# Optimization experiments

Hardware: AMD Instinct MI355X
Metric: run time of the kernel (lower is better)

Reference implementation:

```python
import jax, jax.numpy as jnp
import numpy as np

N_FACTORS = (50, 50, 50)   # vocab factorization, prod = 125000
EMB_STD = (0.5 / 512) ** (1.0 / 3.0)   # per-core std so full embedding std ~= 0.5/embedding_dim
CTX_STD = (1e-6) ** (1.0 / 3.0)


def _tt_gather(core1, core2, core3, idx):
    """idx: flat int array (N,). Cores: (n_k, r_in, m_k, r_out). Returns (N, m1*m2*m3)."""
    n1, n2, n3 = N_FACTORS
    i3 = idx % n3
    i2 = (idx // n3) % n2
    i1 = idx // (n2 * n3)
    N = idx.shape[0]
    g1 = core1[i1][:, 0]                  # (N, m1, r1)  (leading rank is 1)
    g2 = core2[i2]                        # (N, r1, m2, r2)
    res = jnp.einsum('bmr,brns->bmns', g1, g2).reshape(N, -1, g2.shape[-1])  # (N, m1*m2, r2)
    g3 = core3[i3]                        # (N, r2, m3, 1)
    res = jnp.einsum('bmr,brns->bmns', res, g3).reshape(N, -1)               # (N, m1*m2*m3)
    return res


def setup_inputs() -> dict:
    key = jax.random.key(0)
    ks = jax.random.split(key, 8)
    vocab = 125000
    word_indices = jax.random.randint(ks[0], (8192, 1), 0, vocab, dtype=jnp.int64 if jax.config.jax_enable_x64 else jnp.int32)
    context_indices = jax.random.randint(ks[1], (8192, 10), 0, vocab, dtype=jnp.int64 if jax.config.jax_enable_x64 else jnp.int32)
    w_core1 = jax.random.normal(ks[2], (50, 1, 8, 32), dtype=jnp.float32) * EMB_STD
    w_core2 = jax.random.normal(ks[3], (50, 32, 8, 32), dtype=jnp.float32) * EMB_STD
    w_core3 = jax.random.normal(ks[4], (50, 32, 8, 1), dtype=jnp.float32) * EMB_STD
    c_core1 = jax.random.normal(ks[5], (50, 1, 8, 32), dtype=jnp.float32) * CTX_STD
    c_core2 = jax.random.normal(ks[6], (50, 32, 8, 32), dtype=jnp.float32) * CTX_STD
    c_core3 = jax.random.normal(ks[7], (50, 32, 8, 1), dtype=jnp.float32) * CTX_STD
    return {
        'word_indices': word_indices,
        'context_indices': context_indices,
        'w_core1': w_core1, 'w_core2': w_core2, 'w_core3': w_core3,
        'c_core1': c_core1, 'c_core2': c_core2, 'c_core3': c_core3,
    }


def reference(word_indices, context_indices, w_core1, w_core2, w_core3, c_core1, c_core2, c_core3):
    # w = self.w_emb.forward(word_indices)[:, 0, :]
    w = _tt_gather(w_core1, w_core2, w_core3, word_indices[:, 0])          # (B, 512)
    # context_indices is 2-D: flatten, lookup, reshape back
    bs, num = context_indices.shape
    c = _tt_gather(c_core1, c_core2, c_core3, context_indices.reshape(-1)) # (B*num, 512)
    c = c.reshape(bs, num, -1)
    return (w, c)
```

## Files before the change

### kernel.cpp

```cpp
#include <hip/hip_runtime.h>


#define NFAC 50
#define TPAIR 2048
#define NPAIRS 2500
#define NKEYS 5000
#define MAXC 192
#define NWORD 8192
#define NCTX  81920
#define NLOOK (NWORD + NCTX)
#define NBB   ((NLOOK + 255) / 256)

typedef short short8 __attribute__((ext_vector_type(8)));
typedef float f32x4v __attribute__((ext_vector_type(4)));

__device__ __forceinline__ unsigned short f2bf(float f) {
    unsigned u = __builtin_bit_cast(unsigned, f);
    u += 0x7FFFu + ((u >> 16) & 1u);
    return (unsigned short)(u >> 16);
}

__device__ __forceinline__ int pair_of(int idx) {
    const int i3 = idx % NFAC;
    const int i2 = (idx / NFAC) % NFAC;
    return i2 * NFAC + i3;
}


__global__ __launch_bounds__(256) void tt_bucket(
    const int* __restrict__ widx, const int* __restrict__ cidx,
    const float* __restrict__ w1, const float* __restrict__ c1,
    int* __restrict__ hist, unsigned* __restrict__ bucket,
    unsigned short* __restrict__ g1w, unsigned short* __restrict__ g1c)
{
    const int b = blockIdx.x;
    if (b >= NBB) {
        const int g = (b - NBB) * 256 + threadIdx.x;
        if (g < 12800) g1w[g] = f2bf(w1[g]);
        else if (g < 25600) g1c[g - 12800] = f2bf(c1[g - 12800]);
        return;
    }
    const int g = b * 256 + threadIdx.x;
    const int idx = (g < NWORD) ? widx[g] : cidx[g - NWORD];
    const int key = (g < NWORD ? 0 : NPAIRS) + pair_of(idx);
    const int i1  = idx / (NFAC * NFAC);
    const int pos = atomicAdd(&hist[key], 1);
    if (pos < MAXC)
        bucket[(size_t)key * MAXC + pos] = (unsigned)g | ((unsigned)i1 << 17);
}


__global__ __launch_bounds__(256, 8) void tt_group_fused(
    const unsigned* __restrict__ bucket, const int* __restrict__ hist,
    const unsigned short* __restrict__ g1w, const unsigned short* __restrict__ g1c,
    const float* __restrict__ w2, const float* __restrict__ w3,
    const float* __restrict__ c2, const float* __restrict__ c3,
    float* __restrict__ out)
{
    const int B = blockIdx.x;
    const int swz = (B & 7) * (NKEYS / 8) + (B >> 3);
    const int key = (swz & 1) ? ((swz >> 1) + NPAIRS) : (swz >> 1);

    int count = hist[key];
    if (count == 0) return;
    if (count > MAXC) count = MAXC;

    const bool isCtx = key >= NPAIRS;
    const int pair = isCtx ? key - NPAIRS : key;
    const float* core2 = isCtx ? c2 : w2;
    const float* core3 = isCtx ? c3 : w3;
    const unsigned short* g1t = isCtx ? g1c : g1w;
    const unsigned* kb = bucket + (size_t)key * MAXC;
    const int i2 = pair / NFAC, i3 = pair % NFAC;

    __shared__ float g3s[256];
    __shared__ unsigned short tl[TPAIR];
    const int t = threadIdx.x;

    g3s[t] = core3[i3 * 256 + t];
    __syncthreads();
    {
        const int r = t >> 3, n = t & 7;
        const float* g2row = core2 + i2 * 8192 + r * 256 + n * 32;
        float acc[8] = {0.f,0.f,0.f,0.f,0.f,0.f,0.f,0.f};
        #pragma unroll
        for (int s4 = 0; s4 < 8; ++s4) {
            const float4 v = reinterpret_cast<const float4*>(g2row)[s4];
            const float vv[4] = {v.x, v.y, v.z, v.w};
            #pragma unroll
            for (int j = 0; j < 4; ++j) {
                const int s = s4 * 4 + j;
                #pragma unroll
                for (int p = 0; p < 8; ++p)
                    acc[p] += vv[j] * g3s[s * 8 + p];
            }
        }
        #pragma unroll
        for (int p = 0; p < 8; ++p) {
            const int np = n * 8 + p;
            const int flat = (np & 3) * 512 + ((r >> 3) * 16 + (np >> 2)) * 8 + (r & 7);
            tl[flat] = f2bf(acc[p]);
        }
    }
    __syncthreads();

    const int wave = t >> 6;
    const int lane = t & 63;
    const short8 b0 = *reinterpret_cast<const short8*>(&tl[0 * 512 + lane * 8]);
    const short8 b1 = *reinterpret_cast<const short8*>(&tl[1 * 512 + lane * 8]);
    const short8 b2 = *reinterpret_cast<const short8*>(&tl[2 * 512 + lane * 8]);
    const short8 b3 = *reinterpret_cast<const short8*>(&tl[3 * 512 + lane * 8]);

    const int l15 = lane & 15;
    const int kg  = lane >> 4;
    const int sel = (lane >> 3) & 1;
    const int am  = lane & 7;

    const int ntile = (count + 1) >> 1;
    for (int jt = wave; jt < ntile; jt += 4) {
        const int j0 = 2 * jt;
        const bool has2 = (j0 + 1) < count;
        const unsigned pk0 = __builtin_amdgcn_readfirstlane(kb[j0]);
        const unsigned pk1 = has2 ? __builtin_amdgcn_readfirstlane(kb[j0 + 1]) : pk0;
        const int lid0 = pk0 & 0x1FFFF, i10 = pk0 >> 17;
        const int lid1 = pk1 & 0x1FFFF, i11 = pk1 >> 17;

        const short8 a = *reinterpret_cast<const short8*>(
            g1t + (sel ? i11 : i10) * 256 + am * 32 + kg * 8);

        const f32x4v z = {0.f, 0.f, 0.f, 0.f};
        const f32x4v d0 = __builtin_amdgcn_mfma_f32_16x16x32_bf16(a, b0, z, 0, 0, 0);
        const f32x4v d1 = __builtin_amdgcn_mfma_f32_16x16x32_bf16(a, b1, z, 0, 0, 0);
        const f32x4v d2 = __builtin_amdgcn_mfma_f32_16x16x32_bf16(a, b2, z, 0, 0, 0);
        const f32x4v d3 = __builtin_amdgcn_mfma_f32_16x16x32_bf16(a, b3, z, 0, 0, 0);

        float* o0 = out + (size_t)lid0 * 512;
        float* o1 = out + (size_t)lid1 * 512;
        #pragma unroll
        for (int q = 0; q < 4; ++q) {
            const int row = kg * 4 + q;
            const int mm = row & 7;
            float* ob = (row >= 8) ? o1 : o0;
            if (row < 8 || has2) {
                f32x4v v; v[0] = d0[q]; v[1] = d1[q]; v[2] = d2[q]; v[3] = d3[q];
                __builtin_nontemporal_store(v, (f32x4v*)(ob + mm * 64 + 4 * l15));
            }
        }
    }
}


__global__ __launch_bounds__(512) void tt_fused(
    const int* __restrict__ word_idx, const int* __restrict__ ctx_idx,
    const float* __restrict__ w1, const float* __restrict__ w2, const float* __restrict__ w3,
    const float* __restrict__ c1, const float* __restrict__ c2, const float* __restrict__ c3,
    float* __restrict__ out)
{
    const int b = blockIdx.x;
    int idx; const float *k1, *k2, *k3; float* o;
    if (b < NWORD) { idx = word_idx[b]; k1 = w1; k2 = w2; k3 = w3; o = out + (size_t)b * 512; }
    else { const int c = b - NWORD; idx = ctx_idx[c]; k1 = c1; k2 = c2; k3 = c3;
           o = out + (size_t)(NWORD + c) * 512; }
    const int i3 = idx % NFAC;
    const int rem = idx / NFAC;
    const int i2 = rem % NFAC;
    const int i1 = rem / NFAC;

    __shared__ float g3s[256];
    __shared__ float g1s[256];
    __shared__ float Ts[TPAIR];
    const int t = threadIdx.x;
    if (t < 256) g3s[t] = k3[i3 * 256 + t];
    else         g1s[t - 256] = k1[i1 * 256 + (t - 256)];
    __syncthreads();

    {
        const int e0 = t * 4;
        const int r = e0 >> 6, n = (e0 >> 3) & 7, p0 = e0 & 7;
        const float* g2row = k2 + i2 * 8192 + r * 256 + n * 32;
        float acc[4] = {0.f,0.f,0.f,0.f};
        #pragma unroll
        for (int s = 0; s < 32; ++s) {
            const float v = g2row[s];
            #pragma unroll
            for (int j = 0; j < 4; ++j) acc[j] += v * g3s[s * 8 + p0 + j];
        }
        reinterpret_cast<float4*>(Ts + e0)[0] = make_float4(acc[0], acc[1], acc[2], acc[3]);
    }
    __syncthreads();

    const int m = t >> 6, np = t & 63;
    float acc = 0.f;
    #pragma unroll
    for (int r = 0; r < 32; ++r)
        acc += g1s[m * 32 + r] * Ts[r * 64 + np];
    o[m * 64 + np] = acc;
}

extern "C" void kernel_launch(void* const* d_in, const int* in_sizes, int n_in,
                              void* d_out, int out_size, void* d_ws, size_t ws_size,
                              hipStream_t stream) {
    const int*   widx = (const int*)d_in[0];
    const int*   cidx = (const int*)d_in[1];
    const float* w1   = (const float*)d_in[2];
    const float* w2   = (const float*)d_in[3];
    const float* w3   = (const float*)d_in[4];
    const float* c1   = (const float*)d_in[5];
    const float* c2   = (const float*)d_in[6];
    const float* c3   = (const float*)d_in[7];
    float* out = (float*)d_out;

    const size_t need = 2 * 25600 + NKEYS * 4 + (size_t)NKEYS * MAXC * 4;

    if (ws_size >= need) {
        unsigned short* g1wb = (unsigned short*)d_ws;
        unsigned short* g1cb = g1wb + 12800;
        int*      hist   = (int*)(g1cb + 12800);
        unsigned* bucket = (unsigned*)(hist + NKEYS);

        hipMemsetAsync(hist, 0, NKEYS * sizeof(int), stream);
        tt_bucket<<<NBB + 100, 256, 0, stream>>>(widx, cidx, w1, c1,
                                                 hist, bucket, g1wb, g1cb);
        tt_group_fused<<<NKEYS, 256, 0, stream>>>(bucket, hist, g1wb, g1cb,
                                                  w2, w3, c2, c3, out);
    } else {
        tt_fused<<<NLOOK, 512, 0, stream>>>(widx, cidx, w1, w2, w3, c1, c2, c3, out);
    }
}
```

Measured before the change: 65.00 us.

## Compute core2×core3 contraction with bf16 MFMA using pre-converted bf16 cores

The per-pair core2·core3 contraction in the grouped kernel now runs as bf16 MFMA tiles instead of scalar FP32 FMAs. It reads core2 and core3 from bf16 copies that the bucketing kernel writes first, with core3 padded into an MFMA B-operand layout. This removes the scalar inner loop and halves the global bytes read for core2 per group. In exchange the bucketing kernel gets extra blocks and writes about 1.7 MB more workspace, and the intermediate product loses precision because it is rounded to bf16 earlier.

```diff
diff --git a/kernel.cpp b/kernel.cpp
--- a/kernel.cpp
+++ b/kernel.cpp
@@ -10,9 +10,11 @@
 #define NCTX  81920
 #define NLOOK (NWORD + NCTX)
 #define NBB   ((NLOOK + 255) / 256)
+#define NE2   409600
 
 typedef short short8 __attribute__((ext_vector_type(8)));
 typedef float f32x4v __attribute__((ext_vector_type(4)));
+typedef unsigned short us4 __attribute__((ext_vector_type(4)));
 
 __device__ __forceinline__ unsigned short f2bf(float f) {
     unsigned u = __builtin_bit_cast(unsigned, f);
@@ -30,31 +32,61 @@
 __global__ __launch_bounds__(256) void tt_bucket(
     const int* __restrict__ widx, const int* __restrict__ cidx,
     const float* __restrict__ w1, const float* __restrict__ c1,
+    const float* __restrict__ w2, const float* __restrict__ c2,
+    const float* __restrict__ w3, const float* __restrict__ c3,
     int* __restrict__ hist, unsigned* __restrict__ bucket,
-    unsigned short* __restrict__ g1w, unsigned short* __restrict__ g1c)
+    unsigned short* __restrict__ g1w, unsigned short* __restrict__ g1c,
+    unsigned short* __restrict__ g2w, unsigned short* __restrict__ g2c,
+    unsigned short* __restrict__ g3w, unsigned short* __restrict__ g3c)
 {
     const int b = blockIdx.x;
-    if (b >= NBB) {
-        const int g = (b - NBB) * 256 + threadIdx.x;
+    const int t = threadIdx.x;
+    if (b < NBB) {
+        const int g = b * 256 + t;
+        const int idx = (g < NWORD) ? widx[g] : cidx[g - NWORD];
+        const int key = (g < NWORD ? 0 : NPAIRS) + pair_of(idx);
+        const int i1  = idx / (NFAC * NFAC);
+        const int pos = atomicAdd(&hist[key], 1);
+        if (pos < MAXC)
+            bucket[(size_t)key * MAXC + pos] = (unsigned)g | ((unsigned)i1 << 17);
+        return;
+    }
+    if (b < NBB + 800) {
+        const int gid = (b - NBB) * 256 + t;
+        const int e = gid * 4;
+        const float* src; unsigned short* dst; int off;
+        if (e < NE2) { src = w2; dst = g2w; off = e; }
+        else         { src = c2; dst = g2c; off = e - NE2; }
+        const float4 v = *reinterpret_cast<const float4*>(src + off);
+        us4 o; o[0] = f2bf(v.x); o[1] = f2bf(v.y); o[2] = f2bf(v.z); o[3] = f2bf(v.w);
+        *reinterpret_cast<us4*>(dst + off) = o;
+        return;
+    }
+    if (b < NBB + 900) {
+        const int g = (b - NBB - 800) * 256 + t;
         if (g < 12800) g1w[g] = f2bf(w1[g]);
-        else if (g < 25600) g1c[g - 12800] = f2bf(c1[g - 12800]);
+        else           g1c[g - 12800] = f2bf(c1[g - 12800]);
         return;
     }
-    const int g = b * 256 + threadIdx.x;
-    const int idx = (g < NWORD) ? widx[g] : cidx[g - NWORD];
-    const int key = (g < NWORD ? 0 : NPAIRS) + pair_of(idx);
-    const int i1  = idx / (NFAC * NFAC);
-    const int pos = atomicAdd(&hist[key], 1);
-    if (pos < MAXC)
-        bucket[(size_t)key * MAXC + pos] = (unsigned)g | ((unsigned)i1 << 17);
+    {
+        const int g = (b - NBB - 900) * 256 + t;
+        const int tab = g / 25600;
+        const int rem = g - tab * 25600;
+        const int i3 = rem >> 9, le = rem & 511;
+        const int l = le >> 3, j = le & 7;
+        const int col = l & 15, k = 8 * (l >> 4) + j;
+        const float* src = tab ? c3 : w3;
+        unsigned short* dst = tab ? g3c : g3w;
+        dst[i3 * 512 + le] = (col < 8) ? f2bf(src[i3 * 256 + k * 8 + col]) : 0;
+    }
 }
 
 
 __global__ __launch_bounds__(256, 8) void tt_group_fused(
     const unsigned* __restrict__ bucket, const int* __restrict__ hist,
     const unsigned short* __restrict__ g1w, const unsigned short* __restrict__ g1c,
-    const float* __restrict__ w2, const float* __restrict__ w3,
-    const float* __restrict__ c2, const float* __restrict__ c3,
+    const unsigned short* __restrict__ g2w, const unsigned short* __restrict__ g2c,
+    const unsigned short* __restrict__ g3w, const unsigned short* __restrict__ g3c,
     float* __restrict__ out)
 {
     const int B = blockIdx.x;
@@ -67,52 +99,49 @@
 
     const bool isCtx = key >= NPAIRS;
     const int pair = isCtx ? key - NPAIRS : key;
-    const float* core2 = isCtx ? c2 : w2;
-    const float* core3 = isCtx ? c3 : w3;
     const unsigned short* g1t = isCtx ? g1c : g1w;
+    const unsigned short* g2t = isCtx ? g2c : g2w;
+    const unsigned short* g3t = isCtx ? g3c : g3w;
     const unsigned* kb = bucket + (size_t)key * MAXC;
     const int i2 = pair / NFAC, i3 = pair % NFAC;
 
-    __shared__ float g3s[256];
     __shared__ unsigned short tl[TPAIR];
     const int t = threadIdx.x;
-
-    g3s[t] = core3[i3 * 256 + t];
-    __syncthreads();
+    const int wave = t >> 6;
+    const int lane = t & 63;
+    const int l15 = lane & 15;
+    const int kg  = lane >> 4;
+
     {
-        const int r = t >> 3, n = t & 7;
-        const float* g2row = core2 + i2 * 8192 + r * 256 + n * 32;
-        float acc[8] = {0.f,0.f,0.f,0.f,0.f,0.f,0.f,0.f};
+        const short8 bg3 = *reinterpret_cast<const short8*>(g3t + i3 * 512 + lane * 8);
+        const unsigned short* g2p = g2t + i2 * 8192;
         #pragma unroll
-        for (int s4 = 0; s4 < 8; ++s4) {
-            const float4 v = reinterpret_cast<const float4*>(g2row)[s4];
-            const float vv[4] = {v.x, v.y, v.z, v.w};
-            #pragma unroll
-            for (int j = 0; j < 4; ++j) {
-                const int s = s4 * 4 + j;
+        for (int tile = 0; tile < 4; ++tile) {
+            const int rbase = wave * 64 + tile * 16;
+            const short8 a = *reinterpret_cast<const short8*>(
+                g2p + (rbase + l15) * 32 + kg * 8);
+            const f32x4v z = {0.f, 0.f, 0.f, 0.f};
+            const f32x4v d = __builtin_amdgcn_mfma_f32_16x16x32_bf16(a, bg3, z, 0, 0, 0);
+            if (l15 < 8) {
+                const int p = l15;
                 #pragma unroll
-                for (int p = 0; p < 8; ++p)
-                    acc[p] += vv[j] * g3s[s * 8 + p];
+                for (int q = 0; q < 4; ++q) {
+                    const int rn = rbase + kg * 4 + q;
+                    const int r = rn >> 3, n = rn & 7;
+                    const int np = n * 8 + p;
+                    const int flat = (np & 3) * 512 + ((r >> 3) * 16 + (np >> 2)) * 8 + (r & 7);
+                    tl[flat] = f2bf(d[q]);
+                }
             }
         }
-        #pragma unroll
-        for (int p = 0; p < 8; ++p) {
-            const int np = n * 8 + p;
-            const int flat = (np & 3) * 512 + ((r >> 3) * 16 + (np >> 2)) * 8 + (r & 7);
-            tl[flat] = f2bf(acc[p]);
-        }
     }
     __syncthreads();
 
-    const int wave = t >> 6;
-    const int lane = t & 63;
     const short8 b0 = *reinterpret_cast<const short8*>(&tl[0 * 512 + lane * 8]);
     const short8 b1 = *reinterpret_cast<const short8*>(&tl[1 * 512 + lane * 8]);
     const short8 b2 = *reinterpret_cast<const short8*>(&tl[2 * 512 + lane * 8]);
     const short8 b3 = *reinterpret_cast<const short8*>(&tl[3 * 512 + lane * 8]);
 
-    const int l15 = lane & 15;
-    const int kg  = lane >> 4;
     const int sel = (lane >> 3) & 1;
     const int am  = lane & 7;
 
@@ -210,19 +239,24 @@
     const float* c3   = (const float*)d_in[7];
     float* out = (float*)d_out;
 
-    const size_t need = 2 * 25600 + NKEYS * 4 + (size_t)NKEYS * MAXC * 4;
+    const size_t need = 896000 * 2 + NKEYS * 4 + (size_t)NKEYS * MAXC * 4;
 
     if (ws_size >= need) {
         unsigned short* g1wb = (unsigned short*)d_ws;
         unsigned short* g1cb = g1wb + 12800;
-        int*      hist   = (int*)(g1cb + 12800);
+        unsigned short* g2wb = g1cb + 12800;
+        unsigned short* g2cb = g2wb + NE2;
+        unsigned short* g3wb = g2cb + NE2;
+        unsigned short* g3cb = g3wb + 25600;
+        int*      hist   = (int*)(g3cb + 25600);
         unsigned* bucket = (unsigned*)(hist + NKEYS);
 
         hipMemsetAsync(hist, 0, NKEYS * sizeof(int), stream);
-        tt_bucket<<<NBB + 100, 256, 0, stream>>>(widx, cidx, w1, c1,
-                                                 hist, bucket, g1wb, g1cb);
-        tt_group_fused<<<NKEYS, 256, 0, stream>>>(bucket, hist, g1wb, g1cb,
-                                                  w2, w3, c2, c3, out);
+        tt_bucket<<<NBB + 1100, 256, 0, stream>>>(
+            widx, cidx, w1, c1, w2, c2, w3, c3,
+            hist, bucket, g1wb, g1cb, g2wb, g2cb, g3wb, g3cb);
+        tt_group_fused<<<NKEYS, 256, 0, stream>>>(
+            bucket, hist, g1wb, g1cb, g2wb, g2cb, g3wb, g3cb, out);
     } else {
         tt_fused<<<NLOOK, 512, 0, stream>>>(widx, cidx, w1, w2, w3, c1, c2, c3, out);
     }
```

Result: faster. 61.86 us (-4.8%).
